# Kernel tuning notes

Hardware: AMD Instinct MI355X
Metric: run time of the kernel (lower is better)

## Reference

```python
import jax, jax.numpy as jnp
import numpy as np

HEADS = 2
K_HOP = 2
RATIO = 0.8
NEG_SLOPE = 0.01


def seg_softmax(logits, seg, num_seg):
    # torch_geometric.utils.softmax: numerically stable segment softmax
    m = jax.ops.segment_max(logits, seg, num_segments=num_seg)
    e = jnp.exp(logits - m[seg])
    d = jax.ops.segment_sum(e, seg, num_segments=num_seg)
    return e / d[seg]


def _attention(key_value, query, seg, num_seg, Wk, W1, W2, W3):
    # Attention.forward with enable_BN=False; weights stored [in,out] so x@W == torch Linear
    a = key_value @ Wk
    h = jnp.concatenate([a, query, a - query, a * query], axis=-1)  # [N,4H]
    h = jax.nn.leaky_relu(h @ W1, NEG_SLOPE)
    h = jax.nn.leaky_relu(h @ W2, NEG_SLOPE)
    h = jax.nn.leaky_relu(h @ W3, NEG_SLOPE)  # [N,1]
    return seg_softmax(h[:, 0], seg, num_seg)[:, None]  # att_weights [N,1]


def setup_inputs():
    key = jax.random.key(0)
    ks = jax.random.split(key, 10)
    B, n, H, epg = 64, 64, 128, 2048
    N = B * n
    x = jax.random.normal(ks[0], (N, H), jnp.float32)
    src = jax.random.randint(ks[1], (B, epg), 0, n)
    dst = jax.random.randint(ks[2], (B, epg), 0, n)
    off = (jnp.arange(B) * n)[:, None]
    edge_index = jnp.stack([(src + off).reshape(-1), (dst + off).reshape(-1)], 0)
    edge_weight = jax.random.uniform(ks[3], (B * epg,), jnp.float32)
    target_x = jax.random.normal(ks[4], (B, H), jnp.float32)
    batch_ixs = jnp.repeat(jnp.arange(B), n)
    s = lambda i, sh: jax.random.normal(ks[i], sh, jnp.float32) / np.sqrt(sh[-2])
    # index 0=cluster_att, 1=query_att, 2=cluster_att2, 3=query_att2
    att_Wk = s(5, (4, H, H))
    att_W1 = s(6, (4, 4 * H, 2 * H))
    att_W2 = s(7, (4, 2 * H, H))
    att_W3 = s(8, (4, H, 1))
    lin_W = s(9, (HEADS, H, H))
    return dict(x=x, edge_index=edge_index, edge_weight=edge_weight, target_x=target_x,
                batch_ixs=batch_ixs, att_Wk=att_Wk, att_W1=att_W1, att_W2=att_W2,
                att_W3=att_W3, lin_W=lin_W)


def reference(x, edge_index, edge_weight, target_x, batch_ixs, att_Wk, att_W1, att_W2, att_W3, lin_W):
    N, H = x.shape
    B = target_x.shape[0]
    n = N // B
    # ---- gcn_norm with self loops (fill 1.0) ----
    loop = jnp.arange(N)
    row = jnp.concatenate([edge_index[0], loop])
    col = jnp.concatenate([edge_index[1], loop])
    w = jnp.concatenate([edge_weight, jnp.ones((N,), edge_weight.dtype)])
    deg = jax.ops.segment_sum(w, col, num_segments=N)
    dinv = jnp.where(deg > 0, jax.lax.rsqrt(jnp.maximum(deg, 1e-12)), 0.0)
    ew = dinv[row] * w * dinv[col]  # [L]
    # ---- k-hop propagation ----
    def hop(v):
        return jax.ops.segment_sum(v[row] * ew[:, None], col, num_segments=N)
    x_q = x
    for _ in range(K_HOP):
        x_q = hop(x_q)
    qt = target_x[batch_ixs]  # repeat_interleave by per-graph counts (sorted batch)
    # ---- multi-head edge attention (reuse_att_w=True, dropout=0 -> E identical per head) ----
    f1 = _attention(x, x_q, batch_ixs, B, att_Wk[0], att_W1[0], att_W2[0], att_W3[0])
    f2 = _attention(x, qt, batch_ixs, B, att_Wk[1], att_W1[1], att_W2[1], att_W3[1])
    E = jax.nn.leaky_relu(f1[col] + f2[row], NEG_SLOPE)  # [L,1]
    E = seg_softmax(E[:, 0], col, N)[:, None]
    x_c = jnp.zeros_like(x)
    E_g = jnp.zeros((row.shape[0], 1), x.dtype)
    agg = jax.ops.segment_sum(x[row] * E, col, num_segments=N)
    for h in range(HEADS):
        x_c = x_c + jax.nn.leaky_relu(x + agg @ lin_W[h], NEG_SLOPE)
        E_g = E_g + E
    x_c = x_c / HEADS
    E_g = E_g / HEADS
    # ---- second k-hop + cluster scoring ----
    x_q2 = x_c
    for _ in range(K_HOP):
        x_q2 = hop(x_q2)
    g1 = _attention(x_c, x_q2, batch_ixs, B, att_Wk[2], att_W1[2], att_W2[2], att_W3[2])
    g2 = _attention(x_c, qt, batch_ixs, B, att_Wk[3], att_W1[3], att_W2[3], att_W3[3])
    # stack over heads then mean == g1+g2 (same attention modules reused per head)
    cluster_score = seg_softmax((g1 + g2)[:, 0], batch_ixs, B)  # [N]
    # ---- per-graph topk (ratio) ----
    kk = int(np.ceil(RATIO * n))
    _, idx = jax.lax.top_k(cluster_score.reshape(B, n), kk)  # descending, matches PyG topk
    perm = (idx + (jnp.arange(B) * n)[:, None]).reshape(-1)  # [Nk]
    x_out = x[perm] * cluster_score[perm][:, None]
    batch_out = batch_ixs[perm]
    # ---- S^T A S (dense equivalent of SparseTensor triple product) ----
    A_d = jnp.zeros((N, N), x.dtype).at[row, col].add(ew)
    S_d = jnp.zeros((N, N), x.dtype).at[row, col].add(E_g[:, 0])
    S_p = S_d[:, perm]  # S[:, perm] -> [N, Nk]
    A2 = S_p.T @ (A_d @ S_p)  # [Nk, Nk]
    Nk = perm.shape[0]
    A2 = A2.at[jnp.arange(Nk), jnp.arange(Nk)].set(1.0)  # fill_diag(1.0)
    return x_out, A2, batch_out, perm
```

## Files before the change

### kernel.cpp

```cpp
#include <hip/hip_runtime.h>

#define KK 52
#define NKOUT 3328
#define NEG 0.01f

typedef __attribute__((ext_vector_type(8))) __bf16 bf16x8;
typedef __attribute__((ext_vector_type(16))) float floatx16;

__device__ __forceinline__ float lrelu(float v){ return v > 0.f ? v : NEG*v; }

#define SW(r, ko) ((r)*40 + ((ko) ^ ((((r)>>3)&3) << 3)))

__device__ __forceinline__ void split_store8(const float* vv, __bf16* P0, __bf16* P1, __bf16* P2, int addr){
  bf16x8 p1, p2, p3;
  #pragma unroll
  for (int j = 0; j < 8; j++){
    __bf16 b1 = (__bf16)vv[j];
    float r1 = vv[j] - (float)b1;
    __bf16 b2 = (__bf16)r1;
    float r2 = r1 - (float)b2;
    p1[j] = b1; p2[j] = b2; p3[j] = (__bf16)r2;
  }
  *(bf16x8*)(P0 + addr) = p1;
  *(bf16x8*)(P1 + addr) = p2;
  *(bf16x8*)(P2 + addr) = p3;
}

__device__ __forceinline__ void mfma6(const __bf16* A0, const __bf16* A1, const __bf16* A2,
                                      const __bf16* B0, const __bf16* B1, const __bf16* B2,
                                      int aoff, int boff, floatx16* acc){
  bf16x8 a1 = *(const bf16x8*)(A0 + aoff);
  bf16x8 a2 = *(const bf16x8*)(A1 + aoff);
  bf16x8 a3 = *(const bf16x8*)(A2 + aoff);
  bf16x8 b1 = *(const bf16x8*)(B0 + boff);
  bf16x8 b2 = *(const bf16x8*)(B1 + boff);
  bf16x8 b3 = *(const bf16x8*)(B2 + boff);
  floatx16 c = *acc;
  c = __builtin_amdgcn_mfma_f32_32x32x16_bf16(a1,b1,c,0,0,0);
  c = __builtin_amdgcn_mfma_f32_32x32x16_bf16(a1,b2,c,0,0,0);
  c = __builtin_amdgcn_mfma_f32_32x32x16_bf16(a2,b1,c,0,0,0);
  c = __builtin_amdgcn_mfma_f32_32x32x16_bf16(a1,b3,c,0,0,0);
  c = __builtin_amdgcn_mfma_f32_32x32x16_bf16(a3,b1,c,0,0,0);
  c = __builtin_amdgcn_mfma_f32_32x32x16_bf16(a2,b2,c,0,0,0);
  *acc = c;
}

__device__ __forceinline__ void g_gemm(const float* A0, int ldA,
                                       const float* __restrict__ W0, int ldW, int K,
                                       __bf16* pb, floatx16* oA, floatx16* oB){
  __bf16 *As0 = pb, *As1 = pb+2560, *As2 = pb+5120;
  __bf16 *Bs0 = pb+7680, *Bs1 = pb+12800, *Bs2 = pb+17920;
  int tid = threadIdx.x;
  int sar = tid >> 2, sako = (tid & 3)*8;
  int bn = tid & 127, bk = (tid >> 7)*16;
  int wv_ = tid >> 6, L = tid & 63, m = L & 31, half = L >> 5;
  int rA = 32*(wv_ & 1) + m, rB0 = (wv_ >> 1)*32 + m, rB1 = rB0 + 64;
  const float* arow = A0 + (size_t)sar*ldA;
  floatx16 accA, accB;
  #pragma unroll
  for (int i = 0; i < 16; i++){ accA[i] = 0.f; accB[i] = 0.f; }
  float ra[8], wv[16];
  {
    float4 v0 = *(const float4*)(arow + sako);
    float4 v1 = *(const float4*)(arow + sako + 4);
    ra[0]=v0.x; ra[1]=v0.y; ra[2]=v0.z; ra[3]=v0.w; ra[4]=v1.x; ra[5]=v1.y; ra[6]=v1.z; ra[7]=v1.w;
    #pragma unroll
    for (int j = 0; j < 16; j++) wv[j] = W0[(size_t)(bk + j)*ldW + bn];
  }
  for (int k0 = 0; k0 < K; k0 += 32){
    split_store8(ra, As0, As1, As2, SW(sar, sako));
    split_store8(wv,     Bs0, Bs1, Bs2, SW(bn, bk));
    split_store8(wv + 8, Bs0, Bs1, Bs2, SW(bn, bk + 8));
    __syncthreads();
    int k1 = k0 + 32;
    float ra2[8], wv2[16];
    if (k1 < K){
      float4 v0 = *(const float4*)(arow + k1 + sako);
      float4 v1 = *(const float4*)(arow + k1 + sako + 4);
      ra2[0]=v0.x; ra2[1]=v0.y; ra2[2]=v0.z; ra2[3]=v0.w; ra2[4]=v1.x; ra2[5]=v1.y; ra2[6]=v1.z; ra2[7]=v1.w;
      #pragma unroll
      for (int j = 0; j < 16; j++) wv2[j] = W0[(size_t)(k1 + bk + j)*ldW + bn];
    }
    #pragma unroll
    for (int kg = 0; kg < 2; kg++){
      int ko = kg*16 + half*8;
      mfma6(As0,As1,As2, Bs0,Bs1,Bs2, SW(rA,ko), SW(rB0,ko), &accA);
      mfma6(As0,As1,As2, Bs0,Bs1,Bs2, SW(rA,ko), SW(rB1,ko), &accB);
    }
    __syncthreads();
    if (k1 < K){
      #pragma unroll
      for (int j = 0; j < 8; j++) ra[j] = ra2[j];
      #pragma unroll
      for (int j = 0; j < 16; j++) wv[j] = wv2[j];
    }
  }
  *oA = accA; *oB = accB;
}

__device__ __forceinline__ void g_gemm64(const float* __restrict__ A0, int ldA,
                                         const float* __restrict__ W0, int ldW, int K,
                                         __bf16* pb, floatx16* oC){
  __bf16 *As0 = pb, *As1 = pb+2560, *As2 = pb+5120;
  __bf16 *Bs0 = pb+7680, *Bs1 = pb+10240, *Bs2 = pb+12800;
  int tid = threadIdx.x;
  int sar = tid >> 2, sako = (tid & 3)*8;
  int bn = tid & 63, bk = (tid >> 6)*8;
  int wv_ = tid >> 6, L = tid & 63, m = L & 31, half = L >> 5;
  int rA = 32*(wv_ & 1) + m, rB = 32*(wv_ >> 1) + m;
  const float* arow = A0 + (size_t)sar*ldA;
  floatx16 acc;
  #pragma unroll
  for (int i = 0; i < 16; i++) acc[i] = 0.f;
  float ra[8], wv[8];
  {
    float4 v0 = *(const float4*)(arow + sako);
    float4 v1 = *(const float4*)(arow + sako + 4);
    ra[0]=v0.x; ra[1]=v0.y; ra[2]=v0.z; ra[3]=v0.w; ra[4]=v1.x; ra[5]=v1.y; ra[6]=v1.z; ra[7]=v1.w;
    #pragma unroll
    for (int j = 0; j < 8; j++) wv[j] = W0[(size_t)(bk + j)*ldW + bn];
  }
  for (int k0 = 0; k0 < K; k0 += 32){
    split_store8(ra, As0, As1, As2, SW(sar, sako));
    split_store8(wv, Bs0, Bs1, Bs2, SW(bn, bk));
    __syncthreads();
    int k1 = k0 + 32;
    float ra2[8], wv2[8];
    if (k1 < K){
      float4 v0 = *(const float4*)(arow + k1 + sako);
      float4 v1 = *(const float4*)(arow + k1 + sako + 4);
      ra2[0]=v0.x; ra2[1]=v0.y; ra2[2]=v0.z; ra2[3]=v0.w; ra2[4]=v1.x; ra2[5]=v1.y; ra2[6]=v1.z; ra2[7]=v1.w;
      #pragma unroll
      for (int j = 0; j < 8; j++) wv2[j] = W0[(size_t)(k1 + bk + j)*ldW + bn];
    }
    #pragma unroll
    for (int kg = 0; kg < 2; kg++){
      int ko = kg*16 + half*8;
      mfma6(As0,As1,As2, Bs0,Bs1,Bs2, SW(rA,ko), SW(rB,ko), &acc);
    }
    __syncthreads();
    if (k1 < K){
      #pragma unroll
      for (int j = 0; j < 8; j++){ ra[j] = ra2[j]; wv[j] = wv2[j]; }
    }
  }
  *oC = acc;
}

__device__ __forceinline__ void g_gemm_h64(const float* __restrict__ arow, const float* __restrict__ qrow,
                                           const float* __restrict__ W1fz, int colbase,
                                           __bf16* pb, floatx16* oC){
  __bf16 *As0 = pb, *As1 = pb+2560, *As2 = pb+5120;
  __bf16 *Bs0 = pb+7680, *Bs1 = pb+10240, *Bs2 = pb+12800;
  int tid = threadIdx.x;
  int sar = tid >> 2, sako = (tid & 3)*8;
  int bn = tid & 63, bk = (tid >> 6)*8;
  int col = colbase + bn;
  int wv_ = tid >> 6, L = tid & 63, m = L & 31, half = L >> 5;
  int rA = 32*(wv_ & 1) + m, rB = 32*(wv_ >> 1) + m;
  auto loadA = [&](int k0, float* r){
    int seg = k0 >> 7, kl = (k0 & 127) + sako;
    if (seg == 0){
      float4 a0 = *(const float4*)(arow + kl), a1 = *(const float4*)(arow + kl + 4);
      r[0]=a0.x; r[1]=a0.y; r[2]=a0.z; r[3]=a0.w; r[4]=a1.x; r[5]=a1.y; r[6]=a1.z; r[7]=a1.w;
    } else if (seg == 1){
      float4 q0 = *(const float4*)(qrow + kl), q1 = *(const float4*)(qrow + kl + 4);
      r[0]=q0.x; r[1]=q0.y; r[2]=q0.z; r[3]=q0.w; r[4]=q1.x; r[5]=q1.y; r[6]=q1.z; r[7]=q1.w;
    } else {
      float4 a0 = *(const float4*)(arow + kl), a1 = *(const float4*)(arow + kl + 4);
      float4 q0 = *(const float4*)(qrow + kl), q1 = *(const float4*)(qrow + kl + 4);
      r[0]=a0.x*q0.x; r[1]=a0.y*q0.y; r[2]=a0.z*q0.z; r[3]=a0.w*q0.w;
      r[4]=a1.x*q1.x; r[5]=a1.y*q1.y; r[6]=a1.z*q1.z; r[7]=a1.w*q1.w;
    }
  };
  auto loadB = [&](int k0, float* r){
    #pragma unroll
    for (int j = 0; j < 8; j++) r[j] = W1fz[(size_t)(k0 + bk + j)*256 + col];
  };
  floatx16 acc;
  #pragma unroll
  for (int i = 0; i < 16; i++) acc[i] = 0.f;
  float ra[8], wv[8];
  loadA(0, ra); loadB(0, wv);
  for (int k0 = 0; k0 < 384; k0 += 32){
    split_store8(ra, As0, As1, As2, SW(sar, sako));
    split_store8(wv, Bs0, Bs1, Bs2, SW(bn, bk));
    __syncthreads();
    int k1 = k0 + 32;
    float ra2[8], wv2[8];
    if (k1 < 384){ loadA(k1, ra2); loadB(k1, wv2); }
    #pragma unroll
    for (int kg = 0; kg < 2; kg++){
      int ko = kg*16 + half*8;
      mfma6(As0,As1,As2, Bs0,Bs1,Bs2, SW(rA,ko), SW(rB,ko), &acc);
    }
    __syncthreads();
    if (k1 < 384){
      #pragma unroll
      for (int j = 0; j < 8; j++){ ra[j] = ra2[j]; wv[j] = wv2[j]; }
    }
  }
  *oC = acc;
}

__device__ __forceinline__ void c_write(floatx16 accA, floatx16 accB, float* C0, int ldC, int act){
  int tid = threadIdx.x, wv_ = tid >> 6, L = tid & 63, m = L & 31, half = L >> 5;
  int rB0 = (wv_ >> 1)*32 + m, rB1 = rB0 + 64;
  int row0 = 32*(wv_ & 1) + 4*half;
  #pragma unroll
  for (int reg = 0; reg < 16; reg++){
    int row = row0 + (reg & 3) + 8*(reg >> 2);
    float va = accA[reg], vb = accB[reg];
    if (act){ va = lrelu(va); vb = lrelu(vb); }
    C0[(size_t)row*ldC + rB0] = va;
    C0[(size_t)row*ldC + rB1] = vb;
  }
}

__device__ __forceinline__ void c_write64(floatx16 acc, float* C0, int ldC, int act){
  int tid = threadIdx.x, wv_ = tid >> 6, L = tid & 63, m = L & 31, half = L >> 5;
  int col = 32*(wv_ >> 1) + m;
  int row0 = 32*(wv_ & 1) + 4*half;
  #pragma unroll
  for (int reg = 0; reg < 16; reg++){
    int row = row0 + (reg & 3) + 8*(reg >> 2);
    float v = acc[reg];
    if (act) v = lrelu(v);
    C0[(size_t)row*ldC + col] = v;
  }
}

__device__ __forceinline__ void hop2_run(const float* A, const float* VfullL, int ldV,
                                         const float* srcG, float* dstG, int dstOff,
                                         float* Vt, float* Tt, int fbeg, int fend){
  int tid = threadIdx.x;
  int tc = (tid & 31)*2, tf = (tid >> 5)*4;
  for (int f0 = fbeg; f0 < fend; f0 += 32){
    if (!VfullL){
      for (int o = tid; o < 2048; o += 256){
        int r = o >> 5, f = o & 31;
        Vt[o] = srcG[r*128 + f0 + f];
      }
      __syncthreads();
    }
    float a00,a01,a02,a03,a10,a11,a12,a13;
    a00=a01=a02=a03=a10=a11=a12=a13=0.f;
    for (int r = 0; r < 64; r++){
      float x0 = A[r*64 + tc], x1 = A[r*64 + tc + 1];
      float4 v4 = VfullL ? *(const float4*)&VfullL[r*ldV + f0 + tf]
                         : *(const float4*)&Vt[r*32 + tf];
      a00 += x0*v4.x; a01 += x0*v4.y; a02 += x0*v4.z; a03 += x0*v4.w;
      a10 += x1*v4.x; a11 += x1*v4.y; a12 += x1*v4.z; a13 += x1*v4.w;
    }
    *(float4*)&Tt[tc*32 + tf]     = make_float4(a00,a01,a02,a03);
    *(float4*)&Tt[(tc+1)*32 + tf] = make_float4(a10,a11,a12,a13);
    __syncthreads();
    a00=a01=a02=a03=a10=a11=a12=a13=0.f;
    for (int r = 0; r < 64; r++){
      float x0 = A[r*64 + tc], x1 = A[r*64 + tc + 1];
      float4 v4 = *(const float4*)&Tt[r*32 + tf];
      a00 += x0*v4.x; a01 += x0*v4.y; a02 += x0*v4.z; a03 += x0*v4.w;
      a10 += x1*v4.x; a11 += x1*v4.y; a12 += x1*v4.z; a13 += x1*v4.w;
    }
    *(float4*)(dstG + tc*128 + dstOff + f0 + tf)     = make_float4(a00,a01,a02,a03);
    *(float4*)(dstG + (tc+1)*128 + dstOff + f0 + tf) = make_float4(a10,a11,a12,a13);
    __syncthreads();
  }
}

__global__ __launch_bounds__(256) void k_p0(const int* __restrict__ ei, const float* __restrict__ ew,
                                            const float* __restrict__ x, const float* __restrict__ Wk,
                                            const float* __restrict__ W1, const float* __restrict__ linW,
                                            float* A_g, float* M_g, float* xq, float* a_buf, float* W1f,
                                            float* xl0, float* xl1, float* outA2){
  __shared__ __align__(16) char POOL[57856];
  float* pf = (float*)POOL;
  __bf16* pb = (__bf16*)POOL;
  int blk = blockIdx.x, tid = threadIdx.x;
  if (blk < 128){
    int b = blk >> 1, fh = blk & 1;
    float* Ws = pf; float* Mc = pf + 4096; float* dv = pf + 8192;
    for (int i = tid; i < 4096; i += 256){ Ws[i] = 0.f; Mc[i] = 0.f; }
    __syncthreads();
    const int* r0 = ei + b*2048;
    const int* c0 = ei + 64*2048 + b*2048;
    const float* w0 = ew + b*2048;
    int base = b*64;
    for (int e = tid; e < 2048; e += 256){
      int r = r0[e] - base, c = c0[e] - base;
      atomicAdd(&Ws[r*64 + c], w0[e]);
      atomicAdd(&Mc[r*64 + c], 1.f);
    }
    if (tid < 64){ atomicAdd(&Ws[tid*65], 1.f); atomicAdd(&Mc[tid*65], 1.f); }
    __syncthreads();
    if (tid < 64){
      float d = 0.f;
      for (int r = 0; r < 64; r++) d += Ws[r*64 + tid];
      dv[tid] = d > 0.f ? rsqrtf(fmaxf(d, 1e-12f)) : 0.f;
    }
    __syncthreads();
    for (int i = tid; i < 4096; i += 256){
      int r = i >> 6, c = i & 63;
      float a = dv[r]*Ws[i]*dv[c];
      Ws[i] = a;
      if (fh == 0){
        A_g[b*4096 + i] = a;
        M_g[b*4096 + i] = Mc[i];
      }
    }
    __syncthreads();
    hop2_run(Ws, nullptr, 0, x + (size_t)b*8192, xq + (size_t)b*8192, 0, pf + 8256, pf + 10304,
             fh*64, fh*64 + 64);
  } else if (blk < 256){
    int idx = blk - 128, z = idx >> 6, b = idx & 63;
    floatx16 cA, cB;
    g_gemm(x + (size_t)b*8192, 128, Wk + (size_t)z*16384, 128, 128, pb, &cA, &cB);
    c_write(cA, cB, a_buf + (size_t)z*524288 + (size_t)b*8192, 128, 0);
  } else if (blk < 320){
    int idx0 = (blk - 256)*6144;
    for (int i = tid; i < 6144; i += 256){
      int g = idx0 + i;
      int zz = g / 98304;
      int r = g - zz*98304;
      int kr = r >> 8, c = r & 255;
      const float* Wz = W1 + (size_t)zz*131072;
      float v;
      if (kr < 128)       v = Wz[kr*256 + c] + Wz[(kr + 256)*256 + c];
      else if (kr < 256)  v = Wz[kr*256 + c] - Wz[(kr + 128)*256 + c];
      else                v = Wz[(kr + 128)*256 + c];
      W1f[g] = v;
    }
  } else if (blk < 3024){
    float4* p = (float4*)outA2;
    int base = (blk - 320)*1024 + tid;
    #pragma unroll
    for (int i = 0; i < 4; i++) p[base + i*256] = make_float4(0.f,0.f,0.f,0.f);
  } else {
    int idx = blk - 3024, z = idx >> 6, b = idx & 63;
    floatx16 cA, cB;
    g_gemm(x + (size_t)b*8192, 128, linW + (size_t)z*16384, 128, 128, pb, &cA, &cB);
    c_write(cA, cB, (z ? xl1 : xl0) + (size_t)b*8192, 128, 0);
  }
}

__global__ __launch_bounds__(256) void k_h1(const float* __restrict__ a_buf, const float* __restrict__ q0,
                                            const float* __restrict__ tgt, const float* __restrict__ W1fp,
                                            float* h1){
  __shared__ __align__(16) char POOL[30720];
  __bf16* pb = (__bf16*)POOL;
  int blk = blockIdx.x, tid = threadIdx.x;
  int b = blk >> 3, z = (blk >> 2) & 1, nq = blk & 3;
  int sar = tid >> 2;
  const float* arow = a_buf + (size_t)z*524288 + ((size_t)b*64 + sar)*128;
  const float* qrow = z ? (tgt + (size_t)b*128) : (q0 + ((size_t)b*64 + sar)*128);
  floatx16 c;
  g_gemm_h64(arow, qrow, W1fp + (size_t)z*98304, nq*64, pb, &c);
  c_write64(c, h1 + (size_t)z*1048576 + (size_t)b*16384 + nq*64, 256, 1);
}

__global__ __launch_bounds__(256) void k_w2p(const float* __restrict__ h1, const float* __restrict__ W2,
                                             const float* __restrict__ W3, float* __restrict__ lp){
  __shared__ __align__(16) char POOL[30720];
  __shared__ float lgp[128];
  __bf16* pb = (__bf16*)POOL;
  int blk = blockIdx.x, tid = threadIdx.x;
  int b = blk >> 2, z = (blk >> 1) & 1, nh = blk & 1;
  floatx16 c;
  g_gemm64(h1 + (size_t)z*1048576 + (size_t)b*16384, 256,
           W2 + (size_t)z*32768 + nh*64, 128, 256, pb, &c);
  int wv_ = tid >> 6, L = tid & 63, m = L & 31, half = L >> 5;
  int col = 32*(wv_ >> 1) + m;
  float w = W3[z*128 + nh*64 + col];
  float v[16];
  #pragma unroll
  for (int reg = 0; reg < 16; reg++) v[reg] = lrelu(c[reg])*w;
  #pragma unroll
  for (int off = 1; off < 32; off <<= 1)
    #pragma unroll
    for (int reg = 0; reg < 16; reg++) v[reg] += __shfl_xor(v[reg], off);
  if (m == 0){
    #pragma unroll
    for (int reg = 0; reg < 16; reg++) lgp[wv_*32 + half*16 + reg] = v[reg];
  }
  __syncthreads();
  if (tid < 64){
    int row = tid, rh = row >> 5, rem = row & 31;
    int hf = (rem >> 2) & 1, rg = (rem & 3) + 4*(rem >> 3);
    float p = lgp[rh*32 + hf*16 + rg] + lgp[(rh + 2)*32 + hf*16 + rg];
    lp[(z*2 + nh)*4096 + b*64 + row] = p;
  }
}

__global__ __launch_bounds__(256) void k_edgehop(const float* __restrict__ M_g, const float* __restrict__ lp,
                                                 const float* __restrict__ x, const float* __restrict__ xl0g,
                                                 const float* __restrict__ xl1g, const float* __restrict__ A_g,
                                                 float* S_g, float* xcb, float* xq2){
  __shared__ __align__(16) float Mc[4096];
  __shared__ __align__(16) float xh[4096];
  __shared__ __align__(16) float xl0h[4096];
  __shared__ __align__(16) float xl1h[4096];
  __shared__ __align__(16) float Ab[4096];
  __shared__ __align__(16) float Tt[2048];
  __shared__ float f1s[64], f2s[64];
  int blk = blockIdx.x, b = blk >> 1, fh = blk & 1, tid = threadIdx.x;
  int foff = fh*64;
  for (int i = tid; i < 4096; i += 256) Mc[i] = M_g[b*4096 + i];
  for (int o = tid*4; o < 4096; o += 1024){
    int r = o >> 6, f = o & 63;
    *(float4*)&xh[o]   = *(const float4*)(x    + (size_t)b*8192 + r*128 + foff + f);
    *(float4*)&xl0h[o] = *(const float4*)(xl0g + (size_t)b*8192 + r*128 + foff + f);
    *(float4*)&xl1h[o] = *(const float4*)(xl1g + (size_t)b*8192 + r*128 + foff + f);
  }
  if (tid < 128){
    int z = tid >> 6, r = tid & 63;
    float d = lp[(z*2)*4096 + b*64 + r] + lp[(z*2 + 1)*4096 + b*64 + r];
    float l = lrelu(d);
    float mx = l;
    #pragma unroll
    for (int off = 32; off; off >>= 1) mx = fmaxf(mx, __shfl_xor(mx, off));
    float e = expf(l - mx);
    float s = e;
    #pragma unroll
    for (int off = 32; off; off >>= 1) s += __shfl_xor(s, off);
    (z ? f2s : f1s)[r] = e/s;
  }
  __syncthreads();
  {
    int c = tid >> 2, sub = tid & 3;
    float m = -1e30f;
    for (int r = sub; r < 64; r += 4)
      if (Mc[r*64 + c] > 0.f) m = fmaxf(m, lrelu(f1s[c] + f2s[r]));
    m = fmaxf(m, __shfl_xor(m, 1));
    m = fmaxf(m, __shfl_xor(m, 2));
    float s = 0.f;
    for (int r = sub; r < 64; r += 4){
      float mc = Mc[r*64 + c];
      if (mc > 0.f) s += mc*expf(lrelu(f1s[c] + f2s[r]) - m);
    }
    s += __shfl_xor(s, 1);
    s += __shfl_xor(s, 2);
    for (int r = sub; r < 64; r += 4){
      float mc = Mc[r*64 + c];
      float v = 0.f;
      if (mc > 0.f) v = mc*expf(lrelu(f1s[c] + f2s[r]) - m)/s;
      Mc[r*64 + c] = v;
    }
  }
  __syncthreads();
  if (fh == 0)
    for (int i = tid; i < 4096; i += 256) S_g[b*4096 + i] = Mc[i];
  {
    int tc = (tid & 15)*4, tf = (tid >> 4)*4;
    float a0[4][4], a1[4][4];
    #pragma unroll
    for (int i = 0; i < 4; i++)
      #pragma unroll
      for (int j = 0; j < 4; j++){ a0[i][j] = 0.f; a1[i][j] = 0.f; }
    for (int r = 0; r < 64; r++){
      float4 e4 = *(const float4*)&Mc[r*64 + tc];
      float4 p0 = *(const float4*)&xl0h[r*64 + tf];
      float4 p1 = *(const float4*)&xl1h[r*64 + tf];
      float e_[4] = {e4.x,e4.y,e4.z,e4.w};
      float p0_[4] = {p0.x,p0.y,p0.z,p0.w};
      float p1_[4] = {p1.x,p1.y,p1.z,p1.w};
      #pragma unroll
      for (int ci = 0; ci < 4; ci++)
        #pragma unroll
        for (int fj = 0; fj < 4; fj++){
          a0[ci][fj] += e_[ci]*p0_[fj];
          a1[ci][fj] += e_[ci]*p1_[fj];
        }
    }
    __syncthreads();
    #pragma unroll
    for (int ci = 0; ci < 4; ci++){
      int c = tc + ci;
      float4 xv = *(const float4*)&xh[c*64 + tf];
      float4 o;
      o.x = 0.5f*(lrelu(xv.x + a0[ci][0]) + lrelu(xv.x + a1[ci][0]));
      o.y = 0.5f*(lrelu(xv.y + a0[ci][1]) + lrelu(xv.y + a1[ci][1]));
      o.z = 0.5f*(lrelu(xv.z + a0[ci][2]) + lrelu(xv.z + a1[ci][2]));
      o.w = 0.5f*(lrelu(xv.w + a0[ci][3]) + lrelu(xv.w + a1[ci][3]));
      *(float4*)&xh[c*64 + tf] = o;
      *(float4*)(xcb + (size_t)b*8192 + c*128 + foff + tf) = o;
    }
  }
  for (int i = tid*4; i < 4096; i += 1024)
    *(float4*)&Ab[i] = *(const float4*)(A_g + b*4096 + i);
  __syncthreads();
  hop2_run(Ab, xh, 64, nullptr, xq2 + (size_t)b*8192, foff, Tt, Tt, 0, 64);
}

__global__ __launch_bounds__(256) void k_wkg(const float* __restrict__ xcb, const float* __restrict__ Wkg,
                                             float* a_buf){
  __shared__ __align__(16) char POOL[30720];
  __bf16* pb = (__bf16*)POOL;
  int blk = blockIdx.x;
  int b = blk >> 2, z = (blk >> 1) & 1, nh = blk & 1;
  floatx16 c;
  g_gemm64(xcb + (size_t)b*8192, 128, Wkg + (size_t)z*16384 + nh*64, 128, 128, pb, &c);
  c_write64(c, a_buf + (size_t)z*524288 + (size_t)b*8192 + nh*64, 128, 0);
}

__global__ __launch_bounds__(256) void k_A2c(const float* __restrict__ lp, const float* __restrict__ x,
                                             const float* __restrict__ A_g, const float* __restrict__ S_g,
                                             float* outA2, float* outX, float* outB, float* outP){
  __shared__ __align__(16) float At[64*68];
  __shared__ __align__(16) float Sp[64*56];
  __shared__ __align__(16) float Tq[64*56];
  __shared__ int pi[64];
  __shared__ float pv[64];
  int b = blockIdx.x, tid = threadIdx.x;
  if (tid < 64){
    int lane = tid;
    float f[2];
    #pragma unroll
    for (int z = 0; z < 2; z++){
      float d = lp[(z*2)*4096 + b*64 + lane] + lp[(z*2 + 1)*4096 + b*64 + lane];
      float l = lrelu(d);
      float mx = l;
      #pragma unroll
      for (int off = 32; off; off >>= 1) mx = fmaxf(mx, __shfl_xor(mx, off));
      float e = expf(l - mx);
      float sm = e;
      #pragma unroll
      for (int off = 32; off; off >>= 1) sm += __shfl_xor(sm, off);
      f[z] = e/sm;
    }
    float l = f[0] + f[1];
    float m = l;
    #pragma unroll
    for (int off = 32; off; off >>= 1) m = fmaxf(m, __shfl_xor(m, off));
    float e = expf(l - m);
    float sm = e;
    #pragma unroll
    for (int off = 32; off; off >>= 1) sm += __shfl_xor(sm, off);
    float v = e/sm;
    int idx = lane;
    #pragma unroll
    for (int k = 2; k <= 64; k <<= 1){
      #pragma unroll
      for (int j = k >> 1; j > 0; j >>= 1){
        float ov = __shfl_xor(v, j);
        int   oi = __shfl_xor(idx, j);
        bool ascBlock = (lane & k) == 0;
        bool iAmLow   = (lane & j) == 0;
        bool otherPrec = (ov > v) || (ov == v && oi < idx);
        bool take = (ascBlock == iAmLow) ? otherPrec : !otherPrec;
        if (take){ v = ov; idx = oi; }
      }
    }
    pi[lane] = idx; pv[lane] = v;
    if (lane < KK){
      outB[b*KK + lane] = (float)b;
      outP[b*KK + lane] = (float)(b*64 + idx);
    }
  }
  __syncthreads();
  for (int o = tid*4; o < KK*128; o += 1024){
    int j = o >> 7, f = o & 127;
    float4 xv = *(const float4*)(x + ((size_t)b*64 + pi[j])*128 + f);
    float sv = pv[j];
    *(float4*)(outX + (size_t)b*KK*128 + o) = make_float4(xv.x*sv, xv.y*sv, xv.z*sv, xv.w*sv);
  }
  for (int idx = tid; idx < 4096; idx += 256){
    int i = idx >> 6, k = idx & 63;
    At[k*68 + i] = A_g[b*4096 + idx];
  }
  for (int idx = tid; idx < 4096; idx += 256){
    int k = idx >> 6, t = idx & 63;
    if (t < 56) Sp[k*56 + t] = (t < KK) ? S_g[b*4096 + k*64 + pi[t]] : 0.f;
  }
  __syncthreads();
  if (tid < 224){
    int i0 = (tid/14)*4, t0 = (tid % 14)*4;
    float acc[4][4];
    #pragma unroll
    for (int a = 0; a < 4; a++)
      #pragma unroll
      for (int c = 0; c < 4; c++) acc[a][c] = 0.f;
    for (int k = 0; k < 64; k++){
      float4 a4 = *(const float4*)&At[k*68 + i0];
      float4 s4 = *(const float4*)&Sp[k*56 + t0];
      float a_[4] = {a4.x,a4.y,a4.z,a4.w};
      float s_[4] = {s4.x,s4.y,s4.z,s4.w};
      #pragma unroll
      for (int ii = 0; ii < 4; ii++)
        #pragma unroll
        for (int tt = 0; tt < 4; tt++) acc[ii][tt] += a_[ii]*s_[tt];
    }
    #pragma unroll
    for (int ii = 0; ii < 4; ii++)
      *(float4*)&Tq[(i0+ii)*56 + t0] = make_float4(acc[ii][0],acc[ii][1],acc[ii][2],acc[ii][3]);
  }
  __syncthreads();
  if (tid < 169){
    int a0 = (tid/13)*4, t0 = (tid % 13)*4;
    float acc[4][4];
    #pragma unroll
    for (int a = 0; a < 4; a++)
      #pragma unroll
      for (int c = 0; c < 4; c++) acc[a][c] = 0.f;
    for (int i = 0; i < 64; i++){
      float4 s4 = *(const float4*)&Sp[i*56 + a0];
      float4 t4 = *(const float4*)&Tq[i*56 + t0];
      float s_[4] = {s4.x,s4.y,s4.z,s4.w};
      float t_[4] = {t4.x,t4.y,t4.z,t4.w};
      #pragma unroll
      for (int aa = 0; aa < 4; aa++)
        #pragma unroll
        for (int tt = 0; tt < 4; tt++) acc[aa][tt] += s_[aa]*t_[tt];
    }
    #pragma unroll
    for (int aa = 0; aa < 4; aa++){
      int a = a0 + aa;
      float4 o;
      o.x = (a == t0    ) ? 1.f : acc[aa][0];
      o.y = (a == t0 + 1) ? 1.f : acc[aa][1];
      o.z = (a == t0 + 2) ? 1.f : acc[aa][2];
      o.w = (a == t0 + 3) ? 1.f : acc[aa][3];
      *(float4*)(outA2 + (size_t)(b*KK + a)*NKOUT + b*KK + t0) = o;
    }
  }
}

extern "C" void kernel_launch(void* const* d_in, const int* in_sizes, int n_in,
                              void* d_out, int out_size, void* d_ws, size_t ws_size,
                              hipStream_t stream){
  const float* x    = (const float*)d_in[0];
  const int*   ei   = (const int*)d_in[1];
  const float* ew   = (const float*)d_in[2];
  const float* tgt  = (const float*)d_in[3];
  const float* Wk   = (const float*)d_in[5];
  const float* W1   = (const float*)d_in[6];
  const float* W2   = (const float*)d_in[7];
  const float* W3   = (const float*)d_in[8];
  const float* linW = (const float*)d_in[9];
  float* out = (float*)d_out;

  float* wf   = (float*)d_ws;
  float* A_g  = wf;
  float* M_g  = wf + 262144;
  float* S_g  = wf + 524288;
  float* xq   = wf + 786432;
  float* xq2  = wf + 1310720;
  float* xl0  = wf + 1835008;
  float* xcb  = wf + 2359296;
  float* a_buf= wf + 2883584;
  float* h1   = wf + 3932160;
  float* lp   = wf + 6029312;
  float* W1f  = wf + 6045696;
  float* xl1  = wf + 6438912;

  float* outX  = out;
  float* outA2 = out + 425984;
  float* outB  = out + 425984 + 11075584;
  float* outP  = outB + NKOUT;

  k_p0<<<dim3(3152), dim3(256), 0, stream>>>(ei, ew, x, Wk, W1, linW, A_g, M_g, xq, a_buf, W1f,
                                             xl0, xl1, outA2);
  k_h1<<<dim3(512), dim3(256), 0, stream>>>(a_buf, xq, tgt, W1f, h1);
  k_w2p<<<dim3(256), dim3(256), 0, stream>>>(h1, W2, W3, lp);
  k_edgehop<<<dim3(128), dim3(256), 0, stream>>>(M_g, lp, x, xl0, xl1, A_g, S_g, xcb, xq2);
  k_wkg<<<dim3(256), dim3(256), 0, stream>>>(xcb, Wk + 2*16384, a_buf);
  k_h1<<<dim3(512), dim3(256), 0, stream>>>(a_buf, xq2, tgt, W1f + 2*98304, h1);
  k_w2p<<<dim3(256), dim3(256), 0, stream>>>(h1, W2 + 2*32768, W3 + 2*128, lp);
  k_A2c<<<dim3(64), dim3(256), 0, stream>>>(lp, x, A_g, S_g, outA2, outX, outB, outP);
}
```

Before: 211.9 us.

## Fuse all stages into one persistent kernel with per-graph block-group barriers

Replaces the eight-kernel pipeline with a single launch in which each graph owns eight blocks that move through stages, synchronised by spin-wait barriers on global atomic slots. The W1 folding is done on the fly when loading B tiles. The cluster Wk projection is fused into the edge-hop job as register-resident MFMA, with the two half-feature partial products summed when loading the next GEMM. The goal is to remove launch gaps and the intermediate xcb/W1f round trips. The cost is that correctness depends on all 512 blocks being co-resident (launch_bounds 256,2), and spin barriers leave blocks idle during the single-block stages.

```diff
diff --git a/kernel.cpp b/kernel.cpp
--- a/kernel.cpp
+++ b/kernel.cpp
@@ -3,6 +3,7 @@
 #define KK 52
 #define NKOUT 3328
 #define NEG 0.01f
+#define BPG 8
 
 typedef __attribute__((ext_vector_type(8))) __bf16 bf16x8;
 typedef __attribute__((ext_vector_type(16))) float floatx16;
@@ -24,6 +25,19 @@
   *(bf16x8*)(P0 + addr) = p1;
   *(bf16x8*)(P1 + addr) = p2;
   *(bf16x8*)(P2 + addr) = p3;
+}
+
+__device__ __forceinline__ void split8r(const float* vv, bf16x8* q1, bf16x8* q2, bf16x8* q3){
+  bf16x8 p1, p2, p3;
+  #pragma unroll
+  for (int j = 0; j < 8; j++){
+    __bf16 b1 = (__bf16)vv[j];
+    float r1 = vv[j] - (float)b1;
+    __bf16 b2 = (__bf16)r1;
+    float r2 = r1 - (float)b2;
+    p1[j] = b1; p2[j] = b2; p3[j] = (__bf16)r2;
+  }
+  *q1 = p1; *q2 = p2; *q3 = p3;
 }
 
 __device__ __forceinline__ void mfma6(const __bf16* A0, const __bf16* A1, const __bf16* A2,
@@ -45,6 +59,37 @@
   *acc = c;
 }
 
+__device__ __forceinline__ void mfma6r(bf16x8 a1, bf16x8 a2, bf16x8 a3,
+                                       bf16x8 b1, bf16x8 b2, bf16x8 b3, floatx16* acc){
+  floatx16 c = *acc;
+  c = __builtin_amdgcn_mfma_f32_32x32x16_bf16(a1,b1,c,0,0,0);
+  c = __builtin_amdgcn_mfma_f32_32x32x16_bf16(a1,b2,c,0,0,0);
+  c = __builtin_amdgcn_mfma_f32_32x32x16_bf16(a2,b1,c,0,0,0);
+  c = __builtin_amdgcn_mfma_f32_32x32x16_bf16(a1,b3,c,0,0,0);
+  c = __builtin_amdgcn_mfma_f32_32x32x16_bf16(a3,b1,c,0,0,0);
+  c = __builtin_amdgcn_mfma_f32_32x32x16_bf16(a2,b2,c,0,0,0);
+  *acc = c;
+}
+
+__device__ __forceinline__ void bsync(int* slots, int g, int j, int stage){
+  __threadfence();
+  __syncthreads();
+  if (threadIdx.x == 0){
+    __hip_atomic_store(&slots[(g*BPG + j)*32], stage, __ATOMIC_RELAXED, __HIP_MEMORY_SCOPE_AGENT);
+    int base = g*BPG*32;
+    for (;;){
+      int ok = 1;
+      #pragma unroll
+      for (int i = 0; i < BPG; i++)
+        ok &= (__hip_atomic_load(&slots[base + i*32], __ATOMIC_RELAXED, __HIP_MEMORY_SCOPE_AGENT) >= stage);
+      if (ok) break;
+      __builtin_amdgcn_s_sleep(2);
+    }
+  }
+  __syncthreads();
+  __threadfence();
+}
+
 __device__ __forceinline__ void g_gemm(const float* A0, int ldA,
                                        const float* __restrict__ W0, int ldW, int K,
                                        __bf16* pb, floatx16* oA, floatx16* oB){
@@ -147,9 +192,10 @@
   *oC = acc;
 }
 
-__device__ __forceinline__ void g_gemm_h64(const float* __restrict__ arow, const float* __restrict__ qrow,
-                                           const float* __restrict__ W1fz, int colbase,
-                                           __bf16* pb, floatx16* oC){
+__device__ __forceinline__ void g_gemm_h64f(const float* arow, const float* arow2,
+                                            const float* __restrict__ qrow,
+                                            const float* __restrict__ W1z, int colbase,
+                                            __bf16* pb, floatx16* oC){
   __bf16 *As0 = pb, *As1 = pb+2560, *As2 = pb+5120;
   __bf16 *Bs0 = pb+7680, *Bs1 = pb+10240, *Bs2 = pb+12800;
   int tid = threadIdx.x;
@@ -158,24 +204,40 @@
   int col = colbase + bn;
   int wv_ = tid >> 6, L = tid & 63, m = L & 31, half = L >> 5;
   int rA = 32*(wv_ & 1) + m, rB = 32*(wv_ >> 1) + m;
+  auto loadAv = [&](int kl, float* r){
+    float4 a0 = *(const float4*)(arow + kl), a1 = *(const float4*)(arow + kl + 4);
+    if (arow2){
+      float4 c0 = *(const float4*)(arow2 + kl), c1 = *(const float4*)(arow2 + kl + 4);
+      a0 = make_float4(a0.x + c0.x, a0.y + c0.y, a0.z + c0.z, a0.w + c0.w);
+      a1 = make_float4(a1.x + c1.x, a1.y + c1.y, a1.z + c1.z, a1.w + c1.w);
+    }
+    r[0]=a0.x; r[1]=a0.y; r[2]=a0.z; r[3]=a0.w; r[4]=a1.x; r[5]=a1.y; r[6]=a1.z; r[7]=a1.w;
+  };
   auto loadA = [&](int k0, float* r){
     int seg = k0 >> 7, kl = (k0 & 127) + sako;
     if (seg == 0){
-      float4 a0 = *(const float4*)(arow + kl), a1 = *(const float4*)(arow + kl + 4);
-      r[0]=a0.x; r[1]=a0.y; r[2]=a0.z; r[3]=a0.w; r[4]=a1.x; r[5]=a1.y; r[6]=a1.z; r[7]=a1.w;
+      loadAv(kl, r);
     } else if (seg == 1){
       float4 q0 = *(const float4*)(qrow + kl), q1 = *(const float4*)(qrow + kl + 4);
       r[0]=q0.x; r[1]=q0.y; r[2]=q0.z; r[3]=q0.w; r[4]=q1.x; r[5]=q1.y; r[6]=q1.z; r[7]=q1.w;
     } else {
-      float4 a0 = *(const float4*)(arow + kl), a1 = *(const float4*)(arow + kl + 4);
+      float av[8];
+      loadAv(kl, av);
       float4 q0 = *(const float4*)(qrow + kl), q1 = *(const float4*)(qrow + kl + 4);
-      r[0]=a0.x*q0.x; r[1]=a0.y*q0.y; r[2]=a0.z*q0.z; r[3]=a0.w*q0.w;
-      r[4]=a1.x*q1.x; r[5]=a1.y*q1.y; r[6]=a1.z*q1.z; r[7]=a1.w*q1.w;
+      r[0]=av[0]*q0.x; r[1]=av[1]*q0.y; r[2]=av[2]*q0.z; r[3]=av[3]*q0.w;
+      r[4]=av[4]*q1.x; r[5]=av[5]*q1.y; r[6]=av[6]*q1.z; r[7]=av[7]*q1.w;
     }
   };
   auto loadB = [&](int k0, float* r){
     #pragma unroll
-    for (int j = 0; j < 8; j++) r[j] = W1fz[(size_t)(k0 + bk + j)*256 + col];
+    for (int t = 0; t < 8; t++){
+      int kr = k0 + bk + t;
+      float v;
+      if (kr < 128)       v = W1z[kr*256 + col] + W1z[(kr + 256)*256 + col];
+      else if (kr < 256)  v = W1z[kr*256 + col] - W1z[(kr + 128)*256 + col];
+      else                v = W1z[(kr + 128)*256 + col];
+      r[t] = v;
+    }
   };
   floatx16 acc;
   #pragma unroll
@@ -268,109 +330,55 @@
   }
 }
 
-__global__ __launch_bounds__(256) void k_p0(const int* __restrict__ ei, const float* __restrict__ ew,
-                                            const float* __restrict__ x, const float* __restrict__ Wk,
-                                            const float* __restrict__ W1, const float* __restrict__ linW,
-                                            float* A_g, float* M_g, float* xq, float* a_buf, float* W1f,
-                                            float* xl0, float* xl1, float* outA2){
-  __shared__ __align__(16) char POOL[57856];
-  float* pf = (float*)POOL;
-  __bf16* pb = (__bf16*)POOL;
-  int blk = blockIdx.x, tid = threadIdx.x;
-  if (blk < 128){
-    int b = blk >> 1, fh = blk & 1;
-    float* Ws = pf; float* Mc = pf + 4096; float* dv = pf + 8192;
-    for (int i = tid; i < 4096; i += 256){ Ws[i] = 0.f; Mc[i] = 0.f; }
-    __syncthreads();
-    const int* r0 = ei + b*2048;
-    const int* c0 = ei + 64*2048 + b*2048;
-    const float* w0 = ew + b*2048;
-    int base = b*64;
-    for (int e = tid; e < 2048; e += 256){
-      int r = r0[e] - base, c = c0[e] - base;
-      atomicAdd(&Ws[r*64 + c], w0[e]);
-      atomicAdd(&Mc[r*64 + c], 1.f);
-    }
-    if (tid < 64){ atomicAdd(&Ws[tid*65], 1.f); atomicAdd(&Mc[tid*65], 1.f); }
-    __syncthreads();
-    if (tid < 64){
-      float d = 0.f;
-      for (int r = 0; r < 64; r++) d += Ws[r*64 + tid];
-      dv[tid] = d > 0.f ? rsqrtf(fmaxf(d, 1e-12f)) : 0.f;
-    }
-    __syncthreads();
-    for (int i = tid; i < 4096; i += 256){
-      int r = i >> 6, c = i & 63;
-      float a = dv[r]*Ws[i]*dv[c];
-      Ws[i] = a;
-      if (fh == 0){
-        A_g[b*4096 + i] = a;
-        M_g[b*4096 + i] = Mc[i];
-      }
-    }
-    __syncthreads();
-    hop2_run(Ws, nullptr, 0, x + (size_t)b*8192, xq + (size_t)b*8192, 0, pf + 8256, pf + 10304,
-             fh*64, fh*64 + 64);
-  } else if (blk < 256){
-    int idx = blk - 128, z = idx >> 6, b = idx & 63;
-    floatx16 cA, cB;
-    g_gemm(x + (size_t)b*8192, 128, Wk + (size_t)z*16384, 128, 128, pb, &cA, &cB);
-    c_write(cA, cB, a_buf + (size_t)z*524288 + (size_t)b*8192, 128, 0);
-  } else if (blk < 320){
-    int idx0 = (blk - 256)*6144;
-    for (int i = tid; i < 6144; i += 256){
-      int g = idx0 + i;
-      int zz = g / 98304;
-      int r = g - zz*98304;
-      int kr = r >> 8, c = r & 255;
-      const float* Wz = W1 + (size_t)zz*131072;
-      float v;
-      if (kr < 128)       v = Wz[kr*256 + c] + Wz[(kr + 256)*256 + c];
-      else if (kr < 256)  v = Wz[kr*256 + c] - Wz[(kr + 128)*256 + c];
-      else                v = Wz[(kr + 128)*256 + c];
-      W1f[g] = v;
-    }
-  } else if (blk < 3024){
-    float4* p = (float4*)outA2;
-    int base = (blk - 320)*1024 + tid;
-    #pragma unroll
-    for (int i = 0; i < 4; i++) p[base + i*256] = make_float4(0.f,0.f,0.f,0.f);
-  } else {
-    int idx = blk - 3024, z = idx >> 6, b = idx & 63;
-    floatx16 cA, cB;
-    g_gemm(x + (size_t)b*8192, 128, linW + (size_t)z*16384, 128, 128, pb, &cA, &cB);
-    c_write(cA, cB, (z ? xl1 : xl0) + (size_t)b*8192, 128, 0);
-  }
-}
-
-__global__ __launch_bounds__(256) void k_h1(const float* __restrict__ a_buf, const float* __restrict__ q0,
-                                            const float* __restrict__ tgt, const float* __restrict__ W1fp,
-                                            float* h1){
-  __shared__ __align__(16) char POOL[30720];
-  __bf16* pb = (__bf16*)POOL;
-  int blk = blockIdx.x, tid = threadIdx.x;
-  int b = blk >> 3, z = (blk >> 2) & 1, nq = blk & 3;
-  int sar = tid >> 2;
-  const float* arow = a_buf + (size_t)z*524288 + ((size_t)b*64 + sar)*128;
-  const float* qrow = z ? (tgt + (size_t)b*128) : (q0 + ((size_t)b*64 + sar)*128);
-  floatx16 c;
-  g_gemm_h64(arow, qrow, W1fp + (size_t)z*98304, nq*64, pb, &c);
-  c_write64(c, h1 + (size_t)z*1048576 + (size_t)b*16384 + nq*64, 256, 1);
-}
-
-__global__ __launch_bounds__(256) void k_w2p(const float* __restrict__ h1, const float* __restrict__ W2,
-                                             const float* __restrict__ W3, float* __restrict__ lp){
-  __shared__ __align__(16) char POOL[30720];
-  __shared__ float lgp[128];
-  __bf16* pb = (__bf16*)POOL;
-  int blk = blockIdx.x, tid = threadIdx.x;
-  int b = blk >> 2, z = (blk >> 1) & 1, nh = blk & 1;
+__device__ void build_job(int b, int fh, float* pf,
+                          const int* __restrict__ ei, const float* __restrict__ ew,
+                          const float* __restrict__ x, float* A_g, float* M_g, float* xq){
+  int tid = threadIdx.x;
+  float* Ws = pf; float* Mc = pf + 4096; float* dv = pf + 8192;
+  for (int i = tid; i < 4096; i += 256){ Ws[i] = 0.f; Mc[i] = 0.f; }
+  __syncthreads();
+  const int* r0 = ei + b*2048;
+  const int* c0 = ei + 64*2048 + b*2048;
+  const float* w0 = ew + b*2048;
+  int base = b*64;
+  for (int e = tid; e < 2048; e += 256){
+    int r = r0[e] - base, c = c0[e] - base;
+    atomicAdd(&Ws[r*64 + c], w0[e]);
+    atomicAdd(&Mc[r*64 + c], 1.f);
+  }
+  if (tid < 64){ atomicAdd(&Ws[tid*65], 1.f); atomicAdd(&Mc[tid*65], 1.f); }
+  __syncthreads();
+  if (tid < 64){
+    float d = 0.f;
+    for (int r = 0; r < 64; r++) d += Ws[r*64 + tid];
+    dv[tid] = d > 0.f ? rsqrtf(fmaxf(d, 1e-12f)) : 0.f;
+  }
+  __syncthreads();
+  for (int i = tid; i < 4096; i += 256){
+    int r = i >> 6, c = i & 63;
+    float a = dv[r]*Ws[i]*dv[c];
+    Ws[i] = a;
+    if (fh == 0){
+      A_g[b*4096 + i] = a;
+      M_g[b*4096 + i] = Mc[i];
+    }
+  }
+  __syncthreads();
+  hop2_run(Ws, nullptr, 0, x + (size_t)b*8192, xq + (size_t)b*8192, 0, pf + 8256, pf + 10304,
+           fh*64, fh*64 + 64);
+}
+
+__device__ void w2p_job(int b, int z, int nh, int head0, float* pf, __bf16* pb,
+                        const float* __restrict__ h1, const float* __restrict__ W2,
+                        const float* __restrict__ W3, float* __restrict__ lp){
+  float* lgp = pf + 7808;
+  int tid = threadIdx.x;
   floatx16 c;
   g_gemm64(h1 + (size_t)z*1048576 + (size_t)b*16384, 256,
-           W2 + (size_t)z*32768 + nh*64, 128, 256, pb, &c);
+           W2 + (size_t)(head0 + z)*32768 + nh*64, 128, 256, pb, &c);
   int wv_ = tid >> 6, L = tid & 63, m = L & 31, half = L >> 5;
   int col = 32*(wv_ >> 1) + m;
-  float w = W3[z*128 + nh*64 + col];
+  float w = W3[(head0 + z)*128 + nh*64 + col];
   float v[16];
   #pragma unroll
   for (int reg = 0; reg < 16; reg++) v[reg] = lrelu(c[reg])*w;
@@ -391,18 +399,19 @@
   }
 }
 
-__global__ __launch_bounds__(256) void k_edgehop(const float* __restrict__ M_g, const float* __restrict__ lp,
-                                                 const float* __restrict__ x, const float* __restrict__ xl0g,
-                                                 const float* __restrict__ xl1g, const float* __restrict__ A_g,
-                                                 float* S_g, float* xcb, float* xq2){
-  __shared__ __align__(16) float Mc[4096];
-  __shared__ __align__(16) float xh[4096];
-  __shared__ __align__(16) float xl0h[4096];
-  __shared__ __align__(16) float xl1h[4096];
-  __shared__ __align__(16) float Ab[4096];
-  __shared__ __align__(16) float Tt[2048];
-  __shared__ float f1s[64], f2s[64];
-  int blk = blockIdx.x, b = blk >> 1, fh = blk & 1, tid = threadIdx.x;
+__device__ void edgehop_job(int b, int fh, float* pf,
+                            const float* __restrict__ M_g, const float* __restrict__ lp,
+                            const float* __restrict__ x, const float* __restrict__ xl0g,
+                            const float* __restrict__ xl1g, const float* __restrict__ A_g,
+                            const float* __restrict__ Wk,
+                            float* S_g, float* ap, float* xq2){
+  float* Mc   = pf;
+  float* xh   = pf + 4096;
+  float* xl0h = pf + 8192;
+  float* xl1h = pf + 12288;
+  float* f1s  = pf + 16384;
+  float* f2s  = pf + 16448;
+  int tid = threadIdx.x;
   int foff = fh*64;
   for (int i = tid; i < 4096; i += 256) Mc[i] = M_g[b*4096 + i];
   for (int o = tid*4; o < 4096; o += 1024){
@@ -482,35 +491,66 @@
       o.z = 0.5f*(lrelu(xv.z + a0[ci][2]) + lrelu(xv.z + a1[ci][2]));
       o.w = 0.5f*(lrelu(xv.w + a0[ci][3]) + lrelu(xv.w + a1[ci][3]));
       *(float4*)&xh[c*64 + tf] = o;
-      *(float4*)(xcb + (size_t)b*8192 + c*128 + foff + tf) = o;
+    }
+  }
+  __syncthreads();
+  {
+    int wv_ = tid >> 6, L = tid & 63, m = L & 31, half = L >> 5;
+    int rA = 32*(wv_ & 1) + m, rB = 32*(wv_ >> 1) + m;
+    bf16x8 af[4][3];
+    #pragma unroll
+    for (int kg = 0; kg < 4; kg++){
+      int ko = kg*16 + half*8;
+      float av[8];
+      float4 v0 = *(const float4*)&xh[rA*64 + ko];
+      float4 v1 = *(const float4*)&xh[rA*64 + ko + 4];
+      av[0]=v0.x; av[1]=v0.y; av[2]=v0.z; av[3]=v0.w; av[4]=v1.x; av[5]=v1.y; av[6]=v1.z; av[7]=v1.w;
+      split8r(av, &af[kg][0], &af[kg][1], &af[kg][2]);
+    }
+    int row0 = 32*(wv_ & 1) + 4*half;
+    #pragma unroll
+    for (int z = 0; z < 2; z++){
+      const float* Wz = Wk + (size_t)(2 + z)*16384;
+      #pragma unroll
+      for (int nh = 0; nh < 2; nh++){
+        floatx16 acc;
+        #pragma unroll
+        for (int i = 0; i < 16; i++) acc[i] = 0.f;
+        int colB = nh*64 + rB;
+        #pragma unroll
+        for (int kg = 0; kg < 4; kg++){
+          int ko = kg*16 + half*8;
+          float bv[8];
+          #pragma unroll
+          for (int i = 0; i < 8; i++) bv[i] = Wz[(size_t)(foff + ko + i)*128 + colB];
+          bf16x8 b1, b2, b3;
+          split8r(bv, &b1, &b2, &b3);
+          mfma6r(af[kg][0], af[kg][1], af[kg][2], b1, b2, b3, &acc);
+        }
+        float* C0 = ap + (size_t)fh*1048576 + (size_t)z*524288 + (size_t)b*8192 + nh*64;
+        #pragma unroll
+        for (int reg = 0; reg < 16; reg++){
+          int row = row0 + (reg & 3) + 8*(reg >> 2);
+          C0[(size_t)row*128 + rB] = acc[reg];
+        }
+      }
     }
   }
   for (int i = tid*4; i < 4096; i += 1024)
-    *(float4*)&Ab[i] = *(const float4*)(A_g + b*4096 + i);
-  __syncthreads();
-  hop2_run(Ab, xh, 64, nullptr, xq2 + (size_t)b*8192, foff, Tt, Tt, 0, 64);
-}
-
-__global__ __launch_bounds__(256) void k_wkg(const float* __restrict__ xcb, const float* __restrict__ Wkg,
-                                             float* a_buf){
-  __shared__ __align__(16) char POOL[30720];
-  __bf16* pb = (__bf16*)POOL;
-  int blk = blockIdx.x;
-  int b = blk >> 2, z = (blk >> 1) & 1, nh = blk & 1;
-  floatx16 c;
-  g_gemm64(xcb + (size_t)b*8192, 128, Wkg + (size_t)z*16384 + nh*64, 128, 128, pb, &c);
-  c_write64(c, a_buf + (size_t)z*524288 + (size_t)b*8192 + nh*64, 128, 0);
-}
-
-__global__ __launch_bounds__(256) void k_A2c(const float* __restrict__ lp, const float* __restrict__ x,
-                                             const float* __restrict__ A_g, const float* __restrict__ S_g,
-                                             float* outA2, float* outX, float* outB, float* outP){
-  __shared__ __align__(16) float At[64*68];
-  __shared__ __align__(16) float Sp[64*56];
-  __shared__ __align__(16) float Tq[64*56];
-  __shared__ int pi[64];
-  __shared__ float pv[64];
-  int b = blockIdx.x, tid = threadIdx.x;
+    *(float4*)&Mc[i] = *(const float4*)(A_g + b*4096 + i);
+  __syncthreads();
+  hop2_run(Mc, xh, 64, nullptr, xq2 + (size_t)b*8192, foff, xl0h, xl0h, 0, 64);
+}
+
+__device__ void A2c_job(int b, float* pf, const float* __restrict__ lp, const float* __restrict__ x,
+                        const float* __restrict__ A_g, const float* __restrict__ S_g,
+                        float* outA2, float* outX, float* outB, float* outP){
+  float* At = pf;
+  float* Sp = pf + 4352;
+  float* Tq = pf + 7936;
+  int*   pi = (int*)(pf + 11520);
+  float* pv = pf + 11584;
+  int tid = threadIdx.x;
   if (tid < 64){
     int lane = tid;
     float f[2];
@@ -622,6 +662,74 @@
       *(float4*)(outA2 + (size_t)(b*KK + a)*NKOUT + b*KK + t0) = o;
     }
   }
+}
+
+__global__ __launch_bounds__(256, 2) void k_all(const int* __restrict__ ei, const float* __restrict__ ew,
+                                                const float* __restrict__ x, const float* __restrict__ tgt,
+                                                const float* __restrict__ Wk, const float* __restrict__ W1,
+                                                const float* __restrict__ W2, const float* __restrict__ W3,
+                                                const float* __restrict__ linW,
+                                                float* A_g, float* M_g, float* S_g, float* xq, float* xq2,
+                                                float* xl0, float* xl1, float* a_buf, float* h1,
+                                                float* lp, float* ap,
+                                                float* outA2, float* outX, float* outB, float* outP,
+                                                int* slots){
+  __shared__ __align__(16) char POOL[66048];
+  float* pf = (float*)POOL;
+  __bf16* pb = (__bf16*)POOL;
+  int blk = blockIdx.x, tid = threadIdx.x;
+  int g = blk >> 3, j = blk & 7, b = g;
+
+  if (j < 2){
+    build_job(b, j, pf, ei, ew, x, A_g, M_g, xq);
+  } else if (j < 4){
+    int z = j - 2;
+    floatx16 cA, cB;
+    g_gemm(x + (size_t)b*8192, 128, Wk + (size_t)z*16384, 128, 128, pb, &cA, &cB);
+    c_write(cA, cB, a_buf + (size_t)z*524288 + (size_t)b*8192, 128, 0);
+  } else if (j < 6){
+    int z = j - 4;
+    floatx16 cA, cB;
+    g_gemm(x + (size_t)b*8192, 128, linW + (size_t)z*16384, 128, 128, pb, &cA, &cB);
+    c_write(cA, cB, (z ? xl1 : xl0) + (size_t)b*8192, 128, 0);
+  } else {
+    float4* p = (float4*)(outA2 + (size_t)(b*52 + (j - 6)*26)*NKOUT);
+    for (int i = tid; i < 26*NKOUT/4; i += 256) p[i] = make_float4(0.f,0.f,0.f,0.f);
+  }
+  bsync(slots, g, j, 1);
+
+  {
+    int z = j >> 2, nq = j & 3;
+    int sar = tid >> 2;
+    const float* arow = a_buf + (size_t)z*524288 + ((size_t)b*64 + sar)*128;
+    const float* qrow = z ? (tgt + (size_t)b*128) : (xq + ((size_t)b*64 + sar)*128);
+    floatx16 c;
+    g_gemm_h64f(arow, nullptr, qrow, W1 + (size_t)z*131072, nq*64, pb, &c);
+    c_write64(c, h1 + (size_t)z*1048576 + (size_t)b*16384 + nq*64, 256, 1);
+  }
+  bsync(slots, g, j, 2);
+
+  if (j < 4) w2p_job(b, j >> 1, j & 1, 0, pf, pb, h1, W2, W3, lp);
+  bsync(slots, g, j, 3);
+
+  if (j < 2) edgehop_job(b, j, pf, M_g, lp, x, xl0, xl1, A_g, Wk, S_g, ap, xq2);
+  bsync(slots, g, j, 4);
+
+  {
+    int z = j >> 2, nq = j & 3;
+    int sar = tid >> 2;
+    size_t aoff = (size_t)z*524288 + ((size_t)b*64 + sar)*128;
+    const float* qrow = z ? (tgt + (size_t)b*128) : (xq2 + ((size_t)b*64 + sar)*128);
+    floatx16 c;
+    g_gemm_h64f(ap + aoff, ap + 1048576 + aoff, qrow, W1 + (size_t)(2 + z)*131072, nq*64, pb, &c);
+    c_write64(c, h1 + (size_t)z*1048576 + (size_t)b*16384 + nq*64, 256, 1);
+  }
+  bsync(slots, g, j, 5);
+
+  if (j < 4) w2p_job(b, j >> 1, j & 1, 2, pf, pb, h1, W2, W3, lp);
+  bsync(slots, g, j, 6);
+
+  if (j == 0) A2c_job(b, pf, lp, x, A_g, S_g, outA2, outX, outB, outP);
 }
 
 extern "C" void kernel_launch(void* const* d_in, const int* in_sizes, int n_in,
@@ -645,25 +753,20 @@
   float* xq   = wf + 786432;
   float* xq2  = wf + 1310720;
   float* xl0  = wf + 1835008;
-  float* xcb  = wf + 2359296;
+  float* xl1  = wf + 2359296;
   float* a_buf= wf + 2883584;
   float* h1   = wf + 3932160;
   float* lp   = wf + 6029312;
-  float* W1f  = wf + 6045696;
-  float* xl1  = wf + 6438912;
+  float* ap   = wf + 6045696;
+  int*  slots = (int*)(wf + 8142848);
 
   float* outX  = out;
   float* outA2 = out + 425984;
   float* outB  = out + 425984 + 11075584;
   float* outP  = outB + NKOUT;
 
-  k_p0<<<dim3(3152), dim3(256), 0, stream>>>(ei, ew, x, Wk, W1, linW, A_g, M_g, xq, a_buf, W1f,
-                                             xl0, xl1, outA2);
-  k_h1<<<dim3(512), dim3(256), 0, stream>>>(a_buf, xq, tgt, W1f, h1);
-  k_w2p<<<dim3(256), dim3(256), 0, stream>>>(h1, W2, W3, lp);
-  k_edgehop<<<dim3(128), dim3(256), 0, stream>>>(M_g, lp, x, xl0, xl1, A_g, S_g, xcb, xq2);
-  k_wkg<<<dim3(256), dim3(256), 0, stream>>>(xcb, Wk + 2*16384, a_buf);
-  k_h1<<<dim3(512), dim3(256), 0, stream>>>(a_buf, xq2, tgt, W1f + 2*98304, h1);
-  k_w2p<<<dim3(256), dim3(256), 0, stream>>>(h1, W2 + 2*32768, W3 + 2*128, lp);
-  k_A2c<<<dim3(64), dim3(256), 0, stream>>>(lp, x, A_g, S_g, outA2, outX, outB, outP);
-}
+  hipMemsetAsync(slots, 0, 65536, stream);
+  k_all<<<dim3(512), dim3(256), 0, stream>>>(ei, ew, x, tgt, Wk, W1, W2, W3, linW,
+                                             A_g, M_g, S_g, xq, xq2, xl0, xl1, a_buf, h1,
+                                             lp, ap, outA2, outX, outB, outP, slots);
+}
```

Result: slower. 783.3 us (+269.7%).
